# Performance work log

Hardware: AMD Instinct MI355X
Metric: run time of the kernel (lower is better)

## Reference

```python
import jax, jax.numpy as jnp
import numpy as np

EPS_BN = 1e-5
EPS_W = 1e-8


def setup_inputs() -> dict:
    key = jax.random.key(0)
    ks = jax.random.split(key, 6)
    B, N, S, D1, D2 = 8, 8192, 2048, 128, 256
    Cin = D1 + D2  # 384
    return {
        "points_position": jax.random.normal(ks[0], (B, 3, N), jnp.float32),
        "sampled_points_position": jax.random.normal(ks[1], (B, 3, S), jnp.float32),
        "skip_points_feature": jax.random.normal(ks[2], (B, D1, N), jnp.float32),
        "sampled_points_feature": jax.random.normal(ks[3], (B, D2, S), jnp.float32),
        "W1": jax.random.normal(ks[4], (256, Cin), jnp.float32) * 0.05,
        "b1": jnp.zeros((256,), jnp.float32),
        "g1": jnp.ones((256,), jnp.float32),
        "beta1": jnp.zeros((256,), jnp.float32),
        "W2": jax.random.normal(ks[5], (128, 256), jnp.float32) * 0.05,
        "b2": jnp.zeros((128,), jnp.float32),
        "g2": jnp.ones((128,), jnp.float32),
        "beta2": jnp.zeros((128,), jnp.float32),
    }


def _bn_relu(x, g, b):
    # train-mode BatchNorm1d over (batch, points) per channel, x: [B,N,C]
    mean = jnp.mean(x, axis=(0, 1), keepdims=True)
    var = jnp.mean(jnp.square(x - mean), axis=(0, 1), keepdims=True)  # biased var
    return jax.nn.relu((x - mean) * jax.lax.rsqrt(var + EPS_BN) * g + b)


def reference(points_position, sampled_points_position, skip_points_feature,
              sampled_points_feature, W1, b1, g1, beta1, W2, b2, g2, beta2):
    pos = points_position.transpose(0, 2, 1)            # [B,N,3]
    spos = sampled_points_position.transpose(0, 2, 1)   # [B,S,3]
    sfeat = sampled_points_feature.transpose(0, 2, 1)   # [B,S,D2]

    # squared pairwise distance [B,N,S]
    d = (jnp.sum(pos * pos, axis=-1, keepdims=True)
         - 2.0 * jnp.einsum("bnc,bsc->bns", pos, spos)
         + jnp.sum(spos * spos, axis=-1)[:, None, :])

    # 3 nearest neighbors (smallest distances)
    neg_d3, idx = jax.lax.top_k(-d, 3)                  # [B,N,3]
    d3 = -neg_d3
    w = 1.0 / (d3 + EPS_W)
    w = w / jnp.sum(w, axis=-1, keepdims=True)          # [B,N,3]

    gathered = jax.vmap(lambda f, i: f[i])(sfeat, idx)  # [B,N,3,D2]
    interp = jnp.einsum("bnk,bnkd->bnd", w, gathered)   # [B,N,D2]

    feat = jnp.concatenate([skip_points_feature.transpose(0, 2, 1), interp], axis=-1)  # [B,N,D1+D2]

    h = _bn_relu(jnp.einsum("bnc,oc->bno", feat, W1) + b1, g1, beta1)  # [B,N,256]
    h = _bn_relu(jnp.einsum("bnc,oc->bno", h, W2) + b2, g2, beta2)     # [B,N,128]
    return h.transpose(0, 2, 1)                          # [B,128,N]
```

## Files before the change

kernel.cpp:

```cpp
#include <hip/hip_runtime.h>

constexpr int BATCH = 8;
constexpr int NPT   = 8192;
constexpr int NSMP  = 2048;
constexpr int D1C   = 128;
constexpr int D2C   = 256;
constexpr int CIN   = 384;
constexpr int C1    = 256;
constexpr int C2    = 128;
constexpr int BN_TOTAL = BATCH * NPT;

constexpr int BM = 128, BK = 32;
constexpr int NRB = BN_TOTAL / BM;

typedef __bf16 bf16x8 __attribute__((ext_vector_type(8)));
typedef short  s16x8  __attribute__((ext_vector_type(8)));
typedef float  f32x4  __attribute__((ext_vector_type(4)));
typedef unsigned short u16x4 __attribute__((ext_vector_type(4)));

__device__ __forceinline__ unsigned short f2bf(float x) {
  unsigned u = __builtin_bit_cast(unsigned, x);
  u += 0x7fffu + ((u >> 16) & 1u);
  return (unsigned short)(u >> 16);
}
__device__ __forceinline__ float bf2f(unsigned short h) {
  return __builtin_bit_cast(float, (unsigned)h << 16);
}

__device__ __forceinline__ void gld_lds16(const void* g, void* l) {
  __builtin_amdgcn_global_load_lds(
      (const __attribute__((address_space(1))) void*)g,
      (__attribute__((address_space(3))) void*)l, 16, 0, 0);
}

constexpr int PT_T = (NSMP / 32) * (D2C / 32) * BATCH;
constexpr int PT_S = (NPT / 32) * (D1C / 32) * BATCH;
constexpr int PT_M = (C1 * CIN + 255) / 256;

__global__ __launch_bounds__(256) void prep_all(
    const float* __restrict__ sfeat, float* __restrict__ sfeatT,
    const float* __restrict__ skip, unsigned short* __restrict__ featB,
    const float* __restrict__ spos, float* __restrict__ sposI,
    float4* __restrict__ qs4,
    const float* __restrict__ W1, unsigned short* __restrict__ W1h,
    const float* __restrict__ W2, unsigned short* __restrict__ W2h,
    float* __restrict__ stats) {
  __shared__ float tile[32][33];
  int bid = blockIdx.x, tid = threadIdx.x;
  int tx = tid & 31, ty = tid >> 5;
  if (bid < PT_T) {
    int z = bid >> 9;
    int r = bid & 511;
    int c0 = (r & 63) * 32;
    int r0 = (r >> 6) * 32;
    const float* inb = sfeat + (size_t)z * D2C * NSMP;
    float* outb = sfeatT + (size_t)z * NSMP * D2C;
#pragma unroll
    for (int i = 0; i < 32; i += 8)
      tile[ty + i][tx] = inb[(size_t)(r0 + ty + i) * NSMP + c0 + tx];
    __syncthreads();
#pragma unroll
    for (int i = 0; i < 32; i += 8)
      outb[(size_t)(c0 + ty + i) * D2C + r0 + tx] = tile[tx][ty + i];
  } else if (bid < PT_T + PT_S) {
    int id = bid - PT_T;
    int z = id >> 10;
    int r = id & 1023;
    int n0 = (r & 255) * 32;
    int d0 = (r >> 8) * 32;
#pragma unroll
    for (int i = 0; i < 32; i += 8)
      tile[ty + i][tx] = skip[((size_t)z * D1C + d0 + ty + i) * NPT + n0 + tx];
    __syncthreads();
#pragma unroll
    for (int i = 0; i < 32; i += 8) {
      int n = n0 + ty + i;
      featB[((size_t)z * NPT + n) * CIN + d0 + tx] = f2bf(tile[tx][ty + i]);
    }
  } else {
    int g = (bid - PT_T - PT_S) * 256 + tid;
    if (g < 768) stats[g] = 0.f;
    if (g < C1 * CIN) W1h[g] = f2bf(W1[g]);
    if (g < C2 * C1)  W2h[g] = f2bf(W2[g]);
    if (g < BATCH * NSMP) {
      int b = g >> 11, s = g & (NSMP - 1);
      const float* sp = spos + (size_t)b * 3 * NSMP;
      float x = sp[s], y = sp[NSMP + s], z = sp[2 * NSMP + s];
      sposI[(size_t)g * 3 + 0] = x;
      sposI[(size_t)g * 3 + 1] = y;
      sposI[(size_t)g * 3 + 2] = z;
      qs4[g] = make_float4(-2.f * x, -2.f * y, -2.f * z,
                           fmaf(x, x, fmaf(y, y, z * z)));
    }
  }
}

constexpr int KWAVES = 8;
constexpr int SEGK = NSMP / KWAVES;

__device__ __forceinline__ void ins_med3(float kf, float& k0, float& k1,
                                         float& k2, float& k3) {
  float o0 = k0, o1 = k1, o2 = k2;
  k0 = fminf(kf, o0);
  k1 = __builtin_amdgcn_fmed3f(kf, o0, o1);
  k2 = __builtin_amdgcn_fmed3f(kf, o1, o2);
  k3 = __builtin_amdgcn_fmed3f(kf, o2, k3);
}

__device__ __forceinline__ bool dless(double d, int i, double D, int I) {
  return d < D || (d == D && i < I);
}
__device__ __forceinline__ void dins3(double d, int i,
                                      double& b0, double& b1, double& b2,
                                      int& i0, int& i1, int& i2) {
  if (dless(d, i, b2, i2)) {
    if (dless(d, i, b1, i1)) {
      b2 = b1; i2 = i1;
      if (dless(d, i, b0, i0)) { b1 = b0; i1 = i0; b0 = d; i0 = i; }
      else                     { b1 = d; i1 = i; }
    } else { b2 = d; i2 = i; }
  }
}

__global__ __launch_bounds__(512, 4) void knn_all(
    const float* __restrict__ pos,
    const float4* __restrict__ qs4g,
    const float* __restrict__ sposI,
    const float* __restrict__ sfeatT,
    unsigned short* __restrict__ featB) {
  __shared__ float mk[KWAVES][4][4][64];
  __shared__ int   il[256][3];
  __shared__ float wl[256][3];
  __shared__ int   fl[256];
  __shared__ int   fcnt;

  int tid = threadIdx.x;
  int wave = tid >> 6, lane = tid & 63;
  int blk = blockIdx.x;
  int b = blk >> 5;
  int n0 = (blk & 31) << 8;

  if (tid == 0) fcnt = 0;

  const float* pb = pos + (size_t)b * 3 * NPT;
  float px[4], py[4], pz[4], pp[4];
#pragma unroll
  for (int m = 0; m < 4; m++) {
    int n = n0 + (m << 6) + lane;
    px[m] = pb[n]; py[m] = pb[NPT + n]; pz[m] = pb[2 * NPT + n];
    pp[m] = fmaf(px[m], px[m], fmaf(py[m], py[m], pz[m] * pz[m]));
  }

  const float INF = __builtin_inff();
  float k0[4], k1[4], k2[4], k3[4];
#pragma unroll
  for (int m = 0; m < 4; m++) { k0[m] = INF; k1[m] = INF; k2[m] = INF; k3[m] = INF; }

  int s0 = wave * SEGK;
  int tv = 0;
  asm volatile("" : "+v"(tv));
  const float4* qseg = qs4g + (size_t)b * NSMP + s0 + tv;

#define KSTEP4(Q, SS)                                                        \
  {                                                                          \
    _Pragma("unroll")                                                        \
    for (int m_ = 0; m_ < 4; m_++) {                                         \
      float tt = (Q).w + pp[m_];       \
      float d_ = fmaf(px[m_], (Q).x,                                         \
                      fmaf(py[m_], (Q).y, fmaf(pz[m_], (Q).z, tt)));         \
      unsigned ki_ = (__builtin_bit_cast(unsigned, d_) & 0xFFFFF800u) |      \
                     (unsigned)(SS);                                         \
      ins_med3(__builtin_bit_cast(float, ki_), k0[m_], k1[m_], k2[m_], k3[m_]); \
    }                                                                        \
  }

  float4 qa[4], qb[4];
#pragma unroll
  for (int u = 0; u < 4; u++) qa[u] = qseg[u];
#pragma unroll
  for (int u = 0; u < 4; u++) qb[u] = qseg[4 + u];

  for (int t = 0; t < SEGK - 8; t += 8) {
    __builtin_amdgcn_sched_barrier(0);
#pragma unroll
    for (int u = 0; u < 4; u++) KSTEP4(qa[u], s0 + t + u)
    __builtin_amdgcn_sched_barrier(0);
#pragma unroll
    for (int u = 0; u < 4; u++) qa[u] = qseg[t + 8 + u];
    __builtin_amdgcn_sched_barrier(0);
#pragma unroll
    for (int u = 0; u < 4; u++) KSTEP4(qb[u], s0 + t + 4 + u)
    __builtin_amdgcn_sched_barrier(0);
#pragma unroll
    for (int u = 0; u < 4; u++) qb[u] = qseg[t + 12 + u];
  }
  __builtin_amdgcn_sched_barrier(0);
#pragma unroll
  for (int u = 0; u < 4; u++) KSTEP4(qa[u], s0 + SEGK - 8 + u)
#pragma unroll
  for (int u = 0; u < 4; u++) KSTEP4(qb[u], s0 + SEGK - 4 + u)
#undef KSTEP4

#pragma unroll
  for (int m = 0; m < 4; m++) {
    mk[wave][0][m][lane] = k0[m];
    mk[wave][1][m][lane] = k1[m];
    mk[wave][2][m][lane] = k2[m];
    mk[wave][3][m][lane] = k3[m];
  }
  __syncthreads();

  if (tid < 256) {
    int pm = tid >> 6, pl = tid & 63;
    float K0 = INF, K1 = INF, K2 = INF, K3 = INF;
#pragma unroll
    for (int w = 0; w < KWAVES; w++)
#pragma unroll
      for (int sl = 0; sl < 4; sl++)
        ins_med3(mk[w][sl][pm][pl], K0, K1, K2, K3);

    int I0 = (int)(__builtin_bit_cast(unsigned, K0) & 0x7FFu);
    int I1 = (int)(__builtin_bit_cast(unsigned, K1) & 0x7FFu);
    int I2 = (int)(__builtin_bit_cast(unsigned, K2) & 0x7FFu);
    float d2m = __builtin_bit_cast(float, __builtin_bit_cast(unsigned, K2) & 0xFFFFF800u);
    float d3m = __builtin_bit_cast(float, __builtin_bit_cast(unsigned, K3) & 0xFFFFF800u);
    bool flag = (d3m - d2m) < 2e-3f * fmaxf(d3m, 0.f) + 1e-5f;
    if (flag) {
      int slot = atomicAdd(&fcnt, 1);
      fl[slot] = tid;
    }
    int n = n0 + tid;
    const float* q = sposI + (size_t)b * 3 * NSMP;
    double pxd = (double)pb[n], pyd = (double)pb[NPT + n], pzd = (double)pb[2 * NPT + n];
    double dd[3]; int II[3] = {I0, I1, I2};
#pragma unroll
    for (int k = 0; k < 3; k++) {
      double dx = pxd - (double)q[3 * II[k]];
      double dy = pyd - (double)q[3 * II[k] + 1];
      double dz = pzd - (double)q[3 * II[k] + 2];
      dd[k] = dx * dx + dy * dy + dz * dz;
    }
    double w0 = 1.0 / (dd[0] + 1e-8);
    double w1 = 1.0 / (dd[1] + 1e-8);
    double w2 = 1.0 / (dd[2] + 1e-8);
    double inv = 1.0 / (w0 + w1 + w2);
    il[tid][0] = I0; il[tid][1] = I1; il[tid][2] = I2;
    wl[tid][0] = (float)(w0 * inv);
    wl[tid][1] = (float)(w1 * inv);
    wl[tid][2] = (float)(w2 * inv);
  }
  __syncthreads();

  int fc = fcnt;
  for (int t = wave; t < fc; t += KWAVES) {
    int P = fl[t];
    int n = n0 + P;
    double pxd = (double)pb[n], pyd = (double)pb[NPT + n], pzd = (double)pb[2 * NPT + n];
    const float* q = sposI + (size_t)b * 3 * NSMP;
    double b0 = 1e300, b1 = 1e300, b2 = 1e300;
    int i0 = 0x7FFFFFFF, i1 = 0x7FFFFFFF, i2 = 0x7FFFFFFF;
    for (int s = lane; s < NSMP; s += 64) {
      double dx = pxd - (double)q[3 * s];
      double dy = pyd - (double)q[3 * s + 1];
      double dz = pzd - (double)q[3 * s + 2];
      double d = dx * dx + dy * dy + dz * dz;
      dins3(d, s, b0, b1, b2, i0, i1, i2);
    }
#pragma unroll
    for (int m = 1; m < 64; m <<= 1) {
      double o0 = __shfl_xor(b0, m, 64), o1 = __shfl_xor(b1, m, 64), o2 = __shfl_xor(b2, m, 64);
      int    j0 = __shfl_xor(i0, m, 64), j1 = __shfl_xor(i1, m, 64), j2 = __shfl_xor(i2, m, 64);
      dins3(o0, j0, b0, b1, b2, i0, i1, i2);
      dins3(o1, j1, b0, b1, b2, i0, i1, i2);
      dins3(o2, j2, b0, b1, b2, i0, i1, i2);
    }
    if (lane == 0) {
      double w0 = 1.0 / (b0 + 1e-8);
      double w1 = 1.0 / (b1 + 1e-8);
      double w2 = 1.0 / (b2 + 1e-8);
      double inv = 1.0 / (w0 + w1 + w2);
      il[P][0] = i0; il[P][1] = i1; il[P][2] = i2;
      wl[P][0] = (float)(w0 * inv);
      wl[P][1] = (float)(w1 * inv);
      wl[P][2] = (float)(w2 * inv);
    }
  }
  __syncthreads();

  const float* base = sfeatT + (size_t)b * NSMP * D2C;
  for (int i = 0; i < 32; i++) {
    int P = (wave << 5) + i;
    int i0 = il[P][0], i1 = il[P][1], i2 = il[P][2];
    float w0 = wl[P][0], w1 = wl[P][1], w2 = wl[P][2];
    float4 v0 = *(const float4*)&base[(size_t)i0 * D2C + (lane << 2)];
    float4 v1 = *(const float4*)&base[(size_t)i1 * D2C + (lane << 2)];
    float4 v2 = *(const float4*)&base[(size_t)i2 * D2C + (lane << 2)];
    u16x4 o;
    o[0] = f2bf(w0 * v0.x + w1 * v1.x + w2 * v2.x);
    o[1] = f2bf(w0 * v0.y + w1 * v1.y + w2 * v2.y);
    o[2] = f2bf(w0 * v0.z + w1 * v1.z + w2 * v2.z);
    o[3] = f2bf(w0 * v0.w + w1 * v1.w + w2 * v2.w);
    *(u16x4*)&featB[((size_t)b * NPT + n0 + P) * CIN + D1C + (lane << 2)] = o;
  }
}

__global__ __launch_bounds__(256) void gemm1_mw(
    const unsigned short* __restrict__ featB,
    const unsigned short* __restrict__ W1h,
    const float* __restrict__ bias,
    unsigned short* __restrict__ Y1,
    float* __restrict__ sum1,
    float* __restrict__ sumsq1) {
  __shared__ __align__(16) unsigned short As[BM * BK];
  __shared__ __align__(16) unsigned short Bs[BM * BK];
  int tid = threadIdx.x;
  int lane = tid & 63, w = tid >> 6;
  int wr = w >> 1, wc = w & 1;
  int m16 = lane & 15, quad = lane >> 4;
  int cb = blockIdx.x, rb = blockIdx.y;
  int row0 = rb * BM, col0 = cb * BM;
  int srow = lane >> 2, scol8 = (lane & 3) * 8;

  f32x4 acc[4][4];
#pragma unroll
  for (int j = 0; j < 4; j++) {
    float bj = bias[col0 + wc * 64 + j * 16 + m16];
#pragma unroll
    for (int i = 0; i < 4; i++) acc[i][j] = f32x4{bj, bj, bj, bj};
  }

  for (int k0 = 0; k0 < CIN; k0 += BK) {
#pragma unroll
    for (int kq = 0; kq < 2; kq++) {
      int ar = 32 * w + 16 * kq + srow;
      int lb = __builtin_amdgcn_readfirstlane((32 * w + 16 * kq) * BK);
      gld_lds16(&featB[(size_t)(row0 + ar) * CIN + k0 + scol8], &As[lb]);
      gld_lds16(&W1h[(size_t)(col0 + ar) * CIN + k0 + scol8], &Bs[lb]);
    }
    __syncthreads();

    bf16x8 a[4], bb[4];
#pragma unroll
    for (int i = 0; i < 4; i++)
      a[i] = __builtin_bit_cast(bf16x8,
          *(const s16x8*)&As[(wr * 64 + i * 16 + m16) * BK + quad * 8]);
#pragma unroll
    for (int j = 0; j < 4; j++)
      bb[j] = __builtin_bit_cast(bf16x8,
          *(const s16x8*)&Bs[(wc * 64 + j * 16 + m16) * BK + quad * 8]);
#pragma unroll
    for (int i = 0; i < 4; i++)
#pragma unroll
      for (int j = 0; j < 4; j++)
        acc[i][j] = __builtin_amdgcn_mfma_f32_16x16x32_bf16(a[i], bb[j], acc[i][j], 0, 0, 0);
    __syncthreads();
  }

#pragma unroll
  for (int j = 0; j < 4; j++) {
    int col = col0 + wc * 64 + j * 16 + m16;
    float s = 0.f, q = 0.f;
#pragma unroll
    for (int i = 0; i < 4; i++)
#pragma unroll
      for (int r = 0; r < 4; r++) {
        float v = acc[i][j][r];
        Y1[(size_t)(row0 + wr * 64 + i * 16 + quad * 4 + r) * C1 + col] = f2bf(v);
        s += v; q = fmaf(v, v, q);
      }
    s += __shfl_xor(s, 16, 64); s += __shfl_xor(s, 32, 64);
    q += __shfl_xor(q, 16, 64); q += __shfl_xor(q, 32, 64);
    if (quad == 0) {
      atomicAdd(&sum1[col], s);
      atomicAdd(&sumsq1[col], q);
    }
  }
}

__global__ __launch_bounds__(256) void gemm2_mw(
    const unsigned short* __restrict__ Y1,
    const float* __restrict__ g1, const float* __restrict__ beta1,
    const float* __restrict__ sum1, const float* __restrict__ sumsq1,
    const unsigned short* __restrict__ W2h,
    const float* __restrict__ bias,
    unsigned short* __restrict__ Y2,
    float* __restrict__ sum2, float* __restrict__ sumsq2) {
  __shared__ __align__(16) unsigned short As[BM * BK];
  __shared__ __align__(16) unsigned short Bs[BM * BK];
  __shared__ float scs[C1], shs[C1];
  int tid = threadIdx.x;
  int lane = tid & 63, w = tid >> 6;
  int wr = w >> 1, wc = w & 1;
  int m16 = lane & 15, quad = lane >> 4;
  int rb = blockIdx.x;
  int row0 = rb * BM, col0 = 0;
  int srow = lane >> 2, scol8 = (lane & 3) * 8;

  {
    const float invBN = 1.0f / (float)BN_TOTAL;
    float mean = sum1[tid] * invBN;
    float var = sumsq1[tid] * invBN - mean * mean;
    float sc = g1[tid] / sqrtf(var + 1e-5f);
    scs[tid] = sc;
    shs[tid] = beta1[tid] - mean * sc;
  }

  f32x4 acc[4][4];
#pragma unroll
  for (int j = 0; j < 4; j++) {
    float bj = bias[col0 + wc * 64 + j * 16 + m16];
#pragma unroll
    for (int i = 0; i < 4; i++) acc[i][j] = f32x4{bj, bj, bj, bj};
  }
  __syncthreads();

  for (int k0 = 0; k0 < C1; k0 += BK) {
#pragma unroll
    for (int kq = 0; kq < 2; kq++) {
      int ar = 32 * w + 16 * kq + srow;
      int lb = __builtin_amdgcn_readfirstlane((32 * w + 16 * kq) * BK);
      gld_lds16(&W2h[(size_t)(col0 + ar) * C1 + k0 + scol8], &Bs[lb]);
      s16x8 v = *(const s16x8*)&Y1[(size_t)(row0 + ar) * C1 + k0 + scol8];
      unsigned short ov[8];
#pragma unroll
      for (int e = 0; e < 8; e++) {
        float x = bf2f((unsigned short)v[e]);
        float y = fmaxf(fmaf(x, scs[k0 + scol8 + e], shs[k0 + scol8 + e]), 0.f);
        ov[e] = f2bf(y);
      }
      *(s16x8*)&As[ar * BK + scol8] = *(const s16x8*)ov;
    }
    __syncthreads();

    bf16x8 a[4], bb[4];
#pragma unroll
    for (int i = 0; i < 4; i++)
      a[i] = __builtin_bit_cast(bf16x8,
          *(const s16x8*)&As[(wr * 64 + i * 16 + m16) * BK + quad * 8]);
#pragma unroll
    for (int j = 0; j < 4; j++)
      bb[j] = __builtin_bit_cast(bf16x8,
          *(const s16x8*)&Bs[(wc * 64 + j * 16 + m16) * BK + quad * 8]);
#pragma unroll
    for (int i = 0; i < 4; i++)
#pragma unroll
      for (int j = 0; j < 4; j++)
        acc[i][j] = __builtin_amdgcn_mfma_f32_16x16x32_bf16(a[i], bb[j], acc[i][j], 0, 0, 0);
    __syncthreads();
  }

#pragma unroll
  for (int j = 0; j < 4; j++) {
    int col = col0 + wc * 64 + j * 16 + m16;
    float s = 0.f, q = 0.f;
#pragma unroll
    for (int i = 0; i < 4; i++)
#pragma unroll
      for (int r = 0; r < 4; r++) {
        float v = acc[i][j][r];
        Y2[(size_t)(row0 + wr * 64 + i * 16 + quad * 4 + r) * C2 + col] = f2bf(v);
        s += v; q = fmaf(v, v, q);
      }
    s += __shfl_xor(s, 16, 64); s += __shfl_xor(s, 32, 64);
    q += __shfl_xor(q, 16, 64); q += __shfl_xor(q, 32, 64);
    if (quad == 0) {
      atomicAdd(&sum2[col], s);
      atomicAdd(&sumsq2[col], q);
    }
  }
}

__global__ void final_kernel(const unsigned short* __restrict__ Y2,
                             const float* __restrict__ sum2,
                             const float* __restrict__ sumsq2,
                             const float* __restrict__ g2,
                             const float* __restrict__ beta2,
                             float* __restrict__ out) {
  __shared__ float tile[32][33];
  int b = blockIdx.z;
  int n0 = blockIdx.x * 32;
  int c0 = blockIdx.y * 32;
  int tx = threadIdx.x, ty = threadIdx.y;
  int c = c0 + tx;
  const float invBN = 1.0f / (float)BN_TOTAL;
  float mean = sum2[c] * invBN;
  float var = sumsq2[c] * invBN - mean * mean;
  float sc = g2[c] / sqrtf(var + 1e-5f);
  float sh = beta2[c] - mean * sc;
#pragma unroll
  for (int i = 0; i < 32; i += 8) {
    int n = n0 + ty + i;
    float v = bf2f(Y2[((size_t)b * NPT + n) * C2 + c0 + tx]);
    tile[ty + i][tx] = fmaxf(fmaf(v, sc, sh), 0.f);
  }
  __syncthreads();
#pragma unroll
  for (int i = 0; i < 32; i += 8) {
    int cc = c0 + ty + i;
    out[((size_t)b * C2 + cc) * NPT + n0 + tx] = tile[tx][ty + i];
  }
}

extern "C" void kernel_launch(void* const* d_in, const int* in_sizes, int n_in,
                              void* d_out, int out_size, void* d_ws, size_t ws_size,
                              hipStream_t stream) {
  (void)in_sizes; (void)n_in; (void)out_size; (void)ws_size;
  const float* pos   = (const float*)d_in[0];
  const float* spos  = (const float*)d_in[1];
  const float* skip  = (const float*)d_in[2];
  const float* sfeat = (const float*)d_in[3];
  const float* W1    = (const float*)d_in[4];
  const float* b1    = (const float*)d_in[5];
  const float* g1    = (const float*)d_in[6];
  const float* beta1 = (const float*)d_in[7];
  const float* W2    = (const float*)d_in[8];
  const float* b2    = (const float*)d_in[9];
  const float* g2    = (const float*)d_in[10];
  const float* beta2 = (const float*)d_in[11];
  float* out = (float*)d_out;

  float* ws = (float*)d_ws;
  size_t off = 0;
  float* sfeatT  = ws + off; off += (size_t)BATCH * NSMP * D2C;
  unsigned short* featB = (unsigned short*)(ws + off); off += (size_t)BN_TOTAL * CIN / 2;
  unsigned short* Y1    = (unsigned short*)(ws + off); off += (size_t)BN_TOTAL * C1 / 2;
  unsigned short* Y2    = (unsigned short*)(ws + off); off += (size_t)BN_TOTAL * C2 / 2;
  unsigned short* W1h   = (unsigned short*)(ws + off); off += (size_t)C1 * CIN / 2;
  unsigned short* W2h   = (unsigned short*)(ws + off); off += (size_t)C2 * C1 / 2;
  float* sposI   = ws + off; off += (size_t)BATCH * NSMP * 3;
  float4* qs4    = (float4*)(ws + off); off += (size_t)BATCH * NSMP * 4;
  float* stats   = ws + off; off += 1024;
  float* sum1   = stats;
  float* sumsq1 = stats + 256;
  float* sum2   = stats + 512;
  float* sumsq2 = stats + 640;

  prep_all<<<PT_T + PT_S + PT_M, 256, 0, stream>>>(
      sfeat, sfeatT, skip, featB, spos, sposI, qs4, W1, W1h, W2, W2h, stats);

  knn_all<<<BN_TOTAL / 256, 512, 0, stream>>>(pos, qs4, sposI, sfeatT, featB);

  gemm1_mw<<<dim3(C1 / BM, NRB), 256, 0, stream>>>(
      featB, W1h, b1, Y1, sum1, sumsq1);

  gemm2_mw<<<NRB, 256, 0, stream>>>(
      Y1, g1, beta1, sum1, sumsq1, W2h, b2, Y2, sum2, sumsq2);

  final_kernel<<<dim3(NPT / 32, C2 / 32, BATCH), dim3(32, 8), 0, stream>>>(
      Y2, sum2, sumsq2, g2, beta2, out);
}
```

Before: 291.6 us.

## Stage sampled points in LDS via direct global-to-LDS loads in KNN kernel

The KNN kernel now copies each batch's full set of sampled-point float4s into a 32KB shared buffer with global-to-LDS loads, then reads them from LDS instead of using the manually double-buffered global loads. The merge scratch array is aliased onto the same buffer. Block-to-batch mapping is interleaved so concurrent blocks cover different batches, and launch bounds drop the minimum blocks per CU from 4 to 2, reflecting the larger LDS footprint. This trades global-load latency for LDS traffic, an extra barrier and possibly lower occupancy.

Measured after the change: 287.7 us. Within noise of the previous version (-1.3%).

```diff
diff --git a/kernel.cpp b/kernel.cpp
--- a/kernel.cpp
+++ b/kernel.cpp
@@ -122,13 +122,16 @@
   }
 }
 
-__global__ __launch_bounds__(512, 4) void knn_all(
+__global__ __launch_bounds__(512, 2) void knn_all(
     const float* __restrict__ pos,
     const float4* __restrict__ qs4g,
     const float* __restrict__ sposI,
     const float* __restrict__ sfeatT,
     unsigned short* __restrict__ featB) {
-  __shared__ float mk[KWAVES][4][4][64];
+  __shared__ __align__(16) unsigned char smem[NSMP * 16];
+  float4* qs  = (float4*)smem;
+  float*  mkf = (float*)smem;
+#define MKF(w, sl, m, l) mkf[(w) * 1024 + ((sl) * 4 + (m)) * 64 + (l)]
   __shared__ int   il[256][3];
   __shared__ float wl[256][3];
   __shared__ int   fl[256];
@@ -137,8 +140,8 @@
   int tid = threadIdx.x;
   int wave = tid >> 6, lane = tid & 63;
   int blk = blockIdx.x;
-  int b = blk >> 5;
-  int n0 = (blk & 31) << 8;
+  int b = blk & 7;
+  int n0 = (blk >> 3) << 8;
 
   if (tid == 0) fcnt = 0;
 
@@ -157,9 +160,11 @@
   for (int m = 0; m < 4; m++) { k0[m] = INF; k1[m] = INF; k2[m] = INF; k3[m] = INF; }
 
   int s0 = wave * SEGK;
-  int tv = 0;
-  asm volatile("" : "+v"(tv));
-  const float4* qseg = qs4g + (size_t)b * NSMP + s0 + tv;
+  const float4* qsrc = qs4g + (size_t)b * NSMP;
+#pragma unroll
+  for (int r = 0; r < 4; r++)
+    gld_lds16(&qsrc[s0 + r * 64 + lane], &qs[s0 + r * 64]);
+  __syncthreads();
 
 #define KSTEP4(Q, SS)                                                        \
   {                                                                          \
@@ -174,39 +179,21 @@
     }                                                                        \
   }
 
-  float4 qa[4], qb[4];
-#pragma unroll
-  for (int u = 0; u < 4; u++) qa[u] = qseg[u];
-#pragma unroll
-  for (int u = 0; u < 4; u++) qb[u] = qseg[4 + u];
-
-  for (int t = 0; t < SEGK - 8; t += 8) {
-    __builtin_amdgcn_sched_barrier(0);
-#pragma unroll
-    for (int u = 0; u < 4; u++) KSTEP4(qa[u], s0 + t + u)
-    __builtin_amdgcn_sched_barrier(0);
-#pragma unroll
-    for (int u = 0; u < 4; u++) qa[u] = qseg[t + 8 + u];
-    __builtin_amdgcn_sched_barrier(0);
-#pragma unroll
-    for (int u = 0; u < 4; u++) KSTEP4(qb[u], s0 + t + 4 + u)
-    __builtin_amdgcn_sched_barrier(0);
-#pragma unroll
-    for (int u = 0; u < 4; u++) qb[u] = qseg[t + 12 + u];
-  }
-  __builtin_amdgcn_sched_barrier(0);
-#pragma unroll
-  for (int u = 0; u < 4; u++) KSTEP4(qa[u], s0 + SEGK - 8 + u)
-#pragma unroll
-  for (int u = 0; u < 4; u++) KSTEP4(qb[u], s0 + SEGK - 4 + u)
+  for (int t = 0; t < SEGK; t += 8) {
+    float4 qv[8];
+#pragma unroll
+    for (int u = 0; u < 8; u++) qv[u] = qs[s0 + t + u];
+#pragma unroll
+    for (int u = 0; u < 8; u++) KSTEP4(qv[u], s0 + t + u)
+  }
 #undef KSTEP4
 
 #pragma unroll
   for (int m = 0; m < 4; m++) {
-    mk[wave][0][m][lane] = k0[m];
-    mk[wave][1][m][lane] = k1[m];
-    mk[wave][2][m][lane] = k2[m];
-    mk[wave][3][m][lane] = k3[m];
+    MKF(wave, 0, m, lane) = k0[m];
+    MKF(wave, 1, m, lane) = k1[m];
+    MKF(wave, 2, m, lane) = k2[m];
+    MKF(wave, 3, m, lane) = k3[m];
   }
   __syncthreads();
 
@@ -217,7 +204,7 @@
     for (int w = 0; w < KWAVES; w++)
 #pragma unroll
       for (int sl = 0; sl < 4; sl++)
-        ins_med3(mk[w][sl][pm][pl], K0, K1, K2, K3);
+        ins_med3(MKF(w, sl, pm, pl), K0, K1, K2, K3);
 
     int I0 = (int)(__builtin_bit_cast(unsigned, K0) & 0x7FFu);
     int I1 = (int)(__builtin_bit_cast(unsigned, K1) & 0x7FFu);
@@ -302,6 +289,7 @@
     o[3] = f2bf(w0 * v0.w + w1 * v1.w + w2 * v2.w);
     *(u16x4*)&featB[((size_t)b * NPT + n0 + P) * CIN + D1C + (lane << 2)] = o;
   }
+#undef MKF
 }
 
 __global__ __launch_bounds__(256) void gemm1_mw(
```
